# Performance work log

Hardware: AMD Instinct MI355X
Metric: run time of the kernel (lower is better)

Reference implementation:

```python
import jax, jax.numpy as jnp
import numpy as np

B, DIN, E, H, V = 1024, 512, 512, 1024, 4096
MAX_LEN = 32  # max_len=33 with force_eos=True -> 32 decode steps


def setup_inputs() -> dict:
    key = jax.random.key(0)
    ks = jax.random.split(key, 12)
    def u(k, shape, fan_in):
        s = 1.0 / np.sqrt(fan_in)
        return jax.random.uniform(k, shape, jnp.float32, -s, s)
    return {
        "x": jax.random.normal(ks[0], (B, DIN), jnp.float32),
        "W_agent": u(ks[1], (DIN, H), DIN),
        "b_agent": u(ks[2], (H,), DIN),
        "sos_embedding": 0.01 * jax.random.normal(ks[3], (E,), jnp.float32),
        "emb": jax.random.normal(ks[4], (V, E), jnp.float32),
        "W_ih": u(ks[5], (E, H), H),
        "W_hh": u(ks[6], (H, H), H),
        "b_ih": u(ks[7], (H,), H),
        "b_hh": u(ks[8], (H,), H),
        "W_out": u(ks[9], (H, V), H),
        "b_out": u(ks[10], (V,), H),
    }


def reference(x, W_agent, b_agent, sos_embedding, emb, W_ih, W_hh, b_ih, b_hh, W_out, b_out):
    h0 = x @ W_agent + b_agent                      # agent(x): [B, H]
    inp0 = jnp.broadcast_to(sos_embedding, (x.shape[0], E))

    def step(carry, _):
        inp, h = carry
        h = jnp.tanh(inp @ W_ih + h @ W_hh + b_ih + b_hh)   # RNNCell
        logp = jax.nn.log_softmax(h @ W_out + b_out, axis=1)  # [B, V]
        tok = jnp.argmax(logp, axis=1)                      # eval-mode sample
        lp = jnp.take_along_axis(logp, tok[:, None], axis=1)[:, 0]
        ent = -jnp.sum(jnp.exp(logp) * logp, axis=1)
        return (emb[tok], h), (tok, lp, ent)

    (_, _), (seq, lps, ents) = jax.lax.scan(step, (inp0, h0), None, length=MAX_LEN)
    seq = seq.T        # [B, MAX_LEN]
    lps = lps.T
    ents = ents.T
    # force_eos: append zero column
    zf = jnp.zeros((seq.shape[0], 1), jnp.float32)
    sequence = jnp.concatenate([seq, zf.astype(seq.dtype)], axis=1)
    logits = jnp.concatenate([lps, zf], axis=1)
    entropy = jnp.concatenate([ents, zf], axis=1)
    return sequence, logits, entropy
```

## Files before the change

kernel.cpp:

```cpp
#include <hip/hip_runtime.h>
#include <math.h>

#define B_   1024
#define DIN  512
#define EMB  512
#define H_   1024
#define V_   4096
#define TSTEPS 32
#define LEN  33

typedef __attribute__((ext_vector_type(8))) short short8_t;
typedef __attribute__((ext_vector_type(4))) float f32x4;

#define AH_P  131072
#define AI_P  65536
#define B3_P  196608
#define BPO_P 524288

__device__ inline unsigned short bf16_rne(float f) {
  unsigned u = __builtin_bit_cast(unsigned, f);
  u += 0x7FFFu + ((u >> 16) & 1u);
  return (unsigned short)(u >> 16);
}
__device__ inline float bf16_to_f(unsigned short h) {
  unsigned u = ((unsigned)h) << 16;
  return __builtin_bit_cast(float, u);
}
struct S3 { short a, b, c; };
__device__ inline S3 split3(float w) {
  unsigned short h0 = bf16_rne(w);  float r1 = w - bf16_to_f(h0);
  unsigned short h1 = bf16_rne(r1); float r2 = r1 - bf16_to_f(h1);
  S3 r; r.a = (short)h0; r.b = (short)h1; r.c = (short)bf16_rne(r2);
  return r;
}

#define T2MERGE(M1,I1,M2,I2, o1,oi1,o2,oi2)                              \
  if (o1 > M1 || (o1 == M1 && oi1 < I1)) {                               \
    float _n2; int _ni2;                                                 \
    if (M1 > o2 || (M1 == o2 && I1 < oi2)) { _n2 = M1; _ni2 = I1; }      \
    else { _n2 = o2; _ni2 = oi2; }                                       \
    M1 = o1; I1 = oi1; M2 = _n2; I2 = _ni2;                              \
  } else if (o1 > M2 || (o1 == M2 && oi1 < I2)) { M2 = o1; I2 = oi1; }

#define GBT 4
#define GKC 256
__global__ __launch_bounds__(256) void k_gemm(
    float* __restrict__ out,
    const float* __restrict__ A1, int K1, const float* __restrict__ W1,
    const float* __restrict__ A2, int K2, const float* __restrict__ W2,
    const float* __restrict__ b1, const float* __restrict__ b2,
    int do_tanh)
{
  const int N = H_;
  __shared__ float sA[GBT][GKC];
  const int tid = threadIdx.x;
  const int bid = blockIdx.x;
  const int colb = (bid & 7) >> 1;
  const int rowb = ((bid >> 3) << 1) | (bid & 1);
  const int rb  = rowb * GBT;
  const int col = colb * 256 + tid;

  float acc[GBT];
  float bias = b1[col] + (b2 ? b2[col] : 0.0f);
#pragma unroll
  for (int r = 0; r < GBT; ++r) acc[r] = bias;

  const int nch = (K1 + K2) / GKC;
  for (int c = 0; c < nch; ++c) {
    const int kb = c * GKC;
    const float* A; const float* W; int k0, strideA;
    if (kb < K1) { A = A1; W = W1; k0 = kb;      strideA = K1; }
    else         { A = A2; W = W2; k0 = kb - K1; strideA = K2; }
    __syncthreads();
    {
      int r = tid >> 6, kk = (tid & 63) << 2;
      *(float4*)&sA[r][kk] = *(const float4*)(A + (size_t)(rb + r) * strideA + k0 + kk);
    }
    __syncthreads();
    const float* Wp = W + (size_t)k0 * N + col;
#pragma unroll 4
    for (int k = 0; k < GKC; k += 4) {
      float4 a0 = *(const float4*)&sA[0][k];
      float4 a1 = *(const float4*)&sA[1][k];
      float4 a2 = *(const float4*)&sA[2][k];
      float4 a3 = *(const float4*)&sA[3][k];
      float w0 = Wp[(size_t)k * N];
      float w1 = Wp[(size_t)(k + 1) * N];
      float w2 = Wp[(size_t)(k + 2) * N];
      float w3 = Wp[(size_t)(k + 3) * N];
      acc[0] = fmaf(a0.x, w0, acc[0]); acc[1] = fmaf(a1.x, w0, acc[1]);
      acc[2] = fmaf(a2.x, w0, acc[2]); acc[3] = fmaf(a3.x, w0, acc[3]);
      acc[0] = fmaf(a0.y, w1, acc[0]); acc[1] = fmaf(a1.y, w1, acc[1]);
      acc[2] = fmaf(a2.y, w1, acc[2]); acc[3] = fmaf(a3.y, w1, acc[3]);
      acc[0] = fmaf(a0.z, w2, acc[0]); acc[1] = fmaf(a1.z, w2, acc[1]);
      acc[2] = fmaf(a2.z, w2, acc[2]); acc[3] = fmaf(a3.z, w2, acc[3]);
      acc[0] = fmaf(a0.w, w3, acc[0]); acc[1] = fmaf(a1.w, w3, acc[1]);
      acc[2] = fmaf(a2.w, w3, acc[2]); acc[3] = fmaf(a3.w, w3, acc[3]);
    }
  }
#pragma unroll
  for (int r = 0; r < GBT; ++r) {
    float v = acc[r];
    if (do_tanh) v = tanhf(v);
    out[(size_t)(rb + r) * N + col] = v;
  }
}

__global__ __launch_bounds__(256) void k_prepack(
    const float* __restrict__ W, unsigned short* __restrict__ Bp)
{
  int t = blockIdx.x * 256 + threadIdx.x;
  int lane = t & 63;
  int ntg  = (t >> 6) & 255;
  int ks   = t >> 14;
  int col  = ntg * 16 + (lane & 15);
  int krow = ks * 32 + ((lane >> 4) << 3);
  short8_t hv, lv;
#pragma unroll
  for (int j = 0; j < 8; ++j) {
    float w = W[(size_t)(krow + j) * V_ + col];
    unsigned short h = bf16_rne(w);
    hv[j] = (short)h;
    lv[j] = (short)bf16_rne(w - bf16_to_f(h));
  }
  size_t base = ((size_t)ks * 256 + ntg) * 64 + lane;
  short8_t* o = (short8_t*)Bp;
  o[base]         = hv;
  o[base + BPO_P] = lv;
}

__global__ __launch_bounds__(256) void k_packW3(
    const float* __restrict__ Wih, const float* __restrict__ Whh,
    unsigned short* __restrict__ BU)
{
  int t = blockIdx.x * 256 + threadIdx.x;
  int lane = t & 63;
  int ntg  = (t >> 6) & 63;
  int ks   = t >> 12;
  int col  = ntg * 16 + (lane & 15);
  int krow = ks * 32 + ((lane >> 4) << 3);
  short8_t p0, p1, p2;
#pragma unroll
  for (int j = 0; j < 8; ++j) {
    int kr = krow + j;
    float w = (kr < DIN) ? Wih[(size_t)kr * H_ + col]
                         : Whh[(size_t)(kr - DIN) * H_ + col];
    S3 s = split3(w);
    p0[j] = s.a; p1[j] = s.b; p2[j] = s.c;
  }
  short8_t* o = (short8_t*)BU;
  size_t base = ((size_t)ks * 64 + ntg) * 64 + lane;
  o[base] = p0; o[base + B3_P] = p1; o[base + 2 * B3_P] = p2;
}

__global__ __launch_bounds__(256) void k_wtrans(
    const float* __restrict__ W, float* __restrict__ WT)
{
  __shared__ float tile[64][65];
  int kb = (blockIdx.x & 15) * 64;
  int vb = (blockIdx.x >> 4) * 64;
  int t = threadIdx.x;
  {
    int vv = t & 63, k0 = (t >> 6) * 16;
    for (int j = 0; j < 16; ++j)
      tile[k0 + j][vv] = W[(size_t)(kb + k0 + j) * V_ + vb + vv];
  }
  __syncthreads();
  {
    int kk = t & 63, v0 = (t >> 6) * 16;
    for (int j = 0; j < 16; ++j)
      WT[(size_t)(vb + v0 + j) * H_ + kb + kk] = tile[kk][v0 + j];
  }
}

__global__ __launch_bounds__(256) void k_packh(
    const float* __restrict__ h, unsigned short* __restrict__ AU)
{
  int t = blockIdx.x * 256 + threadIdx.x;
  int r = t >> 7, q = t & 127;
  int ks = q >> 2, kg = q & 3;
  int lanep = (r & 15) + (kg << 4);
  int rt = r >> 4;
  const float* src = h + (size_t)r * H_ + q * 8;
  float4 f0 = *(const float4*)src;
  float4 f1 = *(const float4*)(src + 4);
  float f[8] = {f0.x, f0.y, f0.z, f0.w, f1.x, f1.y, f1.z, f1.w};
  short8_t p0, p1, p2;
#pragma unroll
  for (int j = 0; j < 8; ++j) {
    S3 s = split3(f[j]);
    p0[j] = s.a; p1[j] = s.b; p2[j] = s.c;
  }
  short8_t* o = (short8_t*)AU;
  size_t base = (size_t)rt * 2048 + (size_t)ks * 64 + lanep;
  o[base] = p0; o[base + AH_P] = p1; o[base + 2 * AH_P] = p2;
}

__global__ __launch_bounds__(256) void k_sos3(
    const float* __restrict__ sos, unsigned short* __restrict__ AU)
{
  int wid = threadIdx.x >> 6, lane = threadIdx.x & 63;
  int row = blockIdx.x * 4 + wid;
  const float* src = sos + lane * 8;
  float4 f0 = *(const float4*)src;
  float4 f1 = *(const float4*)(src + 4);
  float f[8] = {f0.x, f0.y, f0.z, f0.w, f1.x, f1.y, f1.z, f1.w};
  short8_t p0, p1, p2;
#pragma unroll
  for (int j = 0; j < 8; ++j) {
    S3 s = split3(f[j]);
    p0[j] = s.a; p1[j] = s.b; p2[j] = s.c;
  }
  int ks = lane >> 2, kg = lane & 3;
  int lanep = (row & 15) + (kg << 4);
  int rt = row >> 4;
  short8_t* o = (short8_t*)AU;
  size_t base = (size_t)rt * 1024 + (size_t)ks * 64 + lanep;
  o[base] = p0; o[base + AI_P] = p1; o[base + 2 * AI_P] = p2;
}

__global__ __launch_bounds__(512) void k_rnn(
    const unsigned short* __restrict__ AinpU, const unsigned short* __restrict__ AhU,
    const unsigned short* __restrict__ Bw3U,
    const float* __restrict__ b1, const float* __restrict__ b2,
    float* __restrict__ hout, unsigned short* __restrict__ AhOutU)
{
  __shared__ float sh[64][65];
  const short8_t* Ainp = (const short8_t*)AinpU;
  const short8_t* Ah   = (const short8_t*)AhU;
  const short8_t* Bw3  = (const short8_t*)Bw3U;

  const int bid  = blockIdx.x;
  const int colb = ((bid & 7) << 1) | ((bid >> 3) & 1);
  const int rowb = bid >> 4;
  const int tid  = threadIdx.x, lane = tid & 63, wid = tid >> 6;
  const int wm = (wid >> 1) & 1, wn = wid & 1, kh = wid >> 2;
  const int l15 = lane & 15, lg = lane >> 4;

  f32x4 acc[2][2];
#pragma unroll
  for (int rt = 0; rt < 2; ++rt)
#pragma unroll
    for (int nt = 0; nt < 2; ++nt) {
      int col = colb * 64 + wn * 32 + nt * 16 + l15;
      float b = (kh == 0) ? (b1[col] + b2[col]) : 0.0f;
      acc[rt][nt] = (f32x4){b, b, b, b};
    }

  const int rt0 = rowb * 4 + wm * 2;
  const int ng0 = colb * 4 + wn * 2;
  const int ks0 = kh * 24;

#define RNN_LOAD(A_, B_, KS)                                                   \
  {                                                                            \
    int _ks = (KS);                                                            \
    if (_ks < 16) {                                                            \
      _Pragma("unroll") for (int rt = 0; rt < 2; ++rt)                         \
        _Pragma("unroll") for (int p = 0; p < 3; ++p)                          \
          A_[rt][p] = Ainp[(size_t)p * AI_P + (size_t)(rt0 + rt) * 1024 +      \
                           (size_t)_ks * 64 + lane];                           \
    } else {                                                                   \
      int _h = _ks - 16;                                                       \
      _Pragma("unroll") for (int rt = 0; rt < 2; ++rt)                         \
        _Pragma("unroll") for (int p = 0; p < 3; ++p)                          \
          A_[rt][p] = Ah[(size_t)p * AH_P + (size_t)(rt0 + rt) * 2048 +        \
                         (size_t)_h * 64 + lane];                              \
    }                                                                          \
    _Pragma("unroll") for (int nt = 0; nt < 2; ++nt)                           \
      _Pragma("unroll") for (int p = 0; p < 3; ++p)                            \
        B_[nt][p] = Bw3[(size_t)p * B3_P + (size_t)_ks * 4096 +                \
                        (size_t)(ng0 + nt) * 64 + lane];                       \
  }

  short8_t a[2][3], bb[2][3];
  RNN_LOAD(a, bb, ks0)
#pragma unroll
  for (int i = 0; i < 24; ++i) {
    short8_t an[2][3], bn[2][3];
    if (i < 23) RNN_LOAD(an, bn, ks0 + i + 1)
#pragma unroll
    for (int rt = 0; rt < 2; ++rt)
#pragma unroll
      for (int nt = 0; nt < 2; ++nt) {
        acc[rt][nt] = __builtin_amdgcn_mfma_f32_16x16x32_bf16(a[rt][0], bb[nt][0], acc[rt][nt], 0, 0, 0);
        acc[rt][nt] = __builtin_amdgcn_mfma_f32_16x16x32_bf16(a[rt][0], bb[nt][1], acc[rt][nt], 0, 0, 0);
        acc[rt][nt] = __builtin_amdgcn_mfma_f32_16x16x32_bf16(a[rt][1], bb[nt][0], acc[rt][nt], 0, 0, 0);
        acc[rt][nt] = __builtin_amdgcn_mfma_f32_16x16x32_bf16(a[rt][1], bb[nt][1], acc[rt][nt], 0, 0, 0);
        acc[rt][nt] = __builtin_amdgcn_mfma_f32_16x16x32_bf16(a[rt][0], bb[nt][2], acc[rt][nt], 0, 0, 0);
        acc[rt][nt] = __builtin_amdgcn_mfma_f32_16x16x32_bf16(a[rt][2], bb[nt][0], acc[rt][nt], 0, 0, 0);
      }
    if (i < 23) {
#pragma unroll
      for (int rt = 0; rt < 2; ++rt)
#pragma unroll
        for (int p = 0; p < 3; ++p) { a[rt][p] = an[rt][p]; bb[rt][p] = bn[rt][p]; }
    }
  }
#undef RNN_LOAD

  if (kh == 1) {
#pragma unroll
    for (int rt = 0; rt < 2; ++rt)
#pragma unroll
      for (int nt = 0; nt < 2; ++nt)
#pragma unroll
        for (int r = 0; r < 4; ++r)
          sh[wm * 32 + rt * 16 + lg * 4 + r][wn * 32 + nt * 16 + l15] = acc[rt][nt][r];
  }
  __syncthreads();
  if (kh == 0) {
#pragma unroll
    for (int rt = 0; rt < 2; ++rt)
#pragma unroll
      for (int nt = 0; nt < 2; ++nt)
#pragma unroll
        for (int r = 0; r < 4; ++r) {
          int lr = wm * 32 + rt * 16 + lg * 4 + r;
          int lc = wn * 32 + nt * 16 + l15;
          float v = tanhf(acc[rt][nt][r] + sh[lr][lc]);
          hout[(size_t)(rowb * 64 + lr) * H_ + colb * 64 + lc] = v;
          sh[lr][lc] = v;
        }
  }
  __syncthreads();
  {
    int lr = tid >> 3, q = tid & 7;
    int gk = colb * 64 + q * 8;
    int ks = gk >> 5, kg = (gk >> 3) & 3;
    int gr = rowb * 64 + lr;
    int lanep = (gr & 15) + (kg << 4);
    int rt = gr >> 4;
    short8_t p0, p1, p2;
#pragma unroll
    for (int j = 0; j < 8; ++j) {
      S3 s = split3(sh[lr][q * 8 + j]);
      p0[j] = s.a; p1[j] = s.b; p2[j] = s.c;
    }
    short8_t* o = (short8_t*)AhOutU;
    size_t base = (size_t)rt * 2048 + (size_t)ks * 64 + lanep;
    o[base] = p0; o[base + AH_P] = p1; o[base + 2 * AH_P] = p2;
  }
}

__global__ __launch_bounds__(256) void k_logits3(
    const unsigned short* __restrict__ AhU, const unsigned short* __restrict__ BpU,
    const float* __restrict__ bout, float4* __restrict__ partA,
    float4* __restrict__ partB)
{
  __shared__ float sred[2][2][32][6];
  __shared__ float sbmax[64];
  const short8_t* Ah = (const short8_t*)AhU;
  const short8_t* Bp = (const short8_t*)BpU;

  const int bid  = blockIdx.x;
  const int colb = ((bid & 7) << 2) | ((bid >> 3) & 3);
  const int rowb = bid >> 5;
  const int tid  = threadIdx.x, lane = tid & 63, wid = tid >> 6;
  const int wm = wid >> 1, wn = wid & 1;
  const int l15 = lane & 15, lg = lane >> 4;

  const int colbase = colb * 128 + wn * 64;
  f32x4 acc[2][4];
#pragma unroll
  for (int nt = 0; nt < 4; ++nt) {
    float b = bout[colbase + nt * 16 + l15];
    acc[0][nt] = (f32x4){b, b, b, b};
    acc[1][nt] = acc[0][nt];
  }
  const int rt0 = rowb * 4 + wm * 2;
  const int ng0 = colb * 8 + wn * 4;

#define LG_LOAD(A_, B_, KS)                                                    \
  {                                                                            \
    int _ks = (KS);                                                            \
    _Pragma("unroll") for (int rt = 0; rt < 2; ++rt)                           \
      _Pragma("unroll") for (int p = 0; p < 2; ++p)                            \
        A_[rt][p] = Ah[(size_t)p * AH_P + (size_t)(rt0 + rt) * 2048 +          \
                       (size_t)_ks * 64 + lane];                               \
    _Pragma("unroll") for (int nt = 0; nt < 4; ++nt)                           \
      _Pragma("unroll") for (int p = 0; p < 2; ++p)                            \
        B_[nt][p] = Bp[(size_t)p * BPO_P + ((size_t)_ks * 256 + ng0 + nt) * 64 \
                       + lane];                                                \
  }

  short8_t a[2][2], bb[4][2];
  LG_LOAD(a, bb, 0)
  for (int ks = 0; ks < 32; ++ks) {
    short8_t an[2][2], bn[4][2];
    if (ks < 31) LG_LOAD(an, bn, ks + 1)
#pragma unroll
    for (int rt = 0; rt < 2; ++rt)
#pragma unroll
      for (int nt = 0; nt < 4; ++nt) {
        acc[rt][nt] = __builtin_amdgcn_mfma_f32_16x16x32_bf16(a[rt][0], bb[nt][0], acc[rt][nt], 0, 0, 0);
        acc[rt][nt] = __builtin_amdgcn_mfma_f32_16x16x32_bf16(a[rt][0], bb[nt][1], acc[rt][nt], 0, 0, 0);
        acc[rt][nt] = __builtin_amdgcn_mfma_f32_16x16x32_bf16(a[rt][1], bb[nt][0], acc[rt][nt], 0, 0, 0);
      }
    if (ks < 31) {
#pragma unroll
      for (int rt = 0; rt < 2; ++rt)
#pragma unroll
        for (int p = 0; p < 2; ++p) a[rt][p] = an[rt][p];
#pragma unroll
      for (int nt = 0; nt < 4; ++nt)
#pragma unroll
        for (int p = 0; p < 2; ++p) bb[nt][p] = bn[nt][p];
    }
  }
#undef LG_LOAD

#pragma unroll
  for (int rt = 0; rt < 2; ++rt)
#pragma unroll
    for (int r = 0; r < 4; ++r) {
      float M1 = -1e30f, M2 = -1e30f; int I1 = 0, I2 = 0;
#pragma unroll
      for (int nt = 0; nt < 4; ++nt) {
        float v = acc[rt][nt][r]; int c = colbase + nt * 16 + l15;
        if (v > M1) { M2 = M1; I2 = I1; M1 = v; I1 = c; }
        else if (v > M2) { M2 = v; I2 = c; }
      }
#pragma unroll
      for (int d = 1; d < 16; d <<= 1) {
        float o1 = __shfl_xor(M1, d); int oi1 = __shfl_xor(I1, d);
        float o2 = __shfl_xor(M2, d); int oi2 = __shfl_xor(I2, d);
        T2MERGE(M1, I1, M2, I2, o1, oi1, o2, oi2)
      }
      if (l15 == 0) {
        int rl = rt * 16 + lg * 4 + r;
        sred[wm][wn][rl][0] = M1; sred[wm][wn][rl][1] = (float)I1;
        sred[wm][wn][rl][2] = M2; sred[wm][wn][rl][3] = (float)I2;
      }
    }
  __syncthreads();
  if (tid < 64) {
    int wmm = tid >> 5, rl = tid & 31;
    float M1 = sred[wmm][0][rl][0]; int I1 = (int)sred[wmm][0][rl][1];
    float M2 = sred[wmm][0][rl][2]; int I2 = (int)sred[wmm][0][rl][3];
    float o1 = sred[wmm][1][rl][0]; int oi1 = (int)sred[wmm][1][rl][1];
    float o2 = sred[wmm][1][rl][2]; int oi2 = (int)sred[wmm][1][rl][3];
    T2MERGE(M1, I1, M2, I2, o1, oi1, o2, oi2)
    int row = rowb * 64 + wmm * 32 + rl;
    partA[(size_t)row * 32 + colb] = make_float4(M1, (float)I1, M2, (float)I2);
    sbmax[wmm * 32 + rl] = M1;
  }
  __syncthreads();
#pragma unroll
  for (int rt = 0; rt < 2; ++rt)
#pragma unroll
    for (int r = 0; r < 4; ++r) {
      float m = sbmax[wm * 32 + rt * 16 + lg * 4 + r];
      float s = 0.f, tsum = 0.f;
#pragma unroll
      for (int nt = 0; nt < 4; ++nt) {
        float d = acc[rt][nt][r] - m;
        float e = expf(d);
        s += e; tsum += d * e;
      }
#pragma unroll
      for (int d = 1; d < 16; d <<= 1) { s += __shfl_xor(s, d); tsum += __shfl_xor(tsum, d); }
      if (l15 == 0) {
        int rl = rt * 16 + lg * 4 + r;
        sred[wm][wn][rl][4] = s; sred[wm][wn][rl][5] = tsum;
      }
    }
  __syncthreads();
  if (tid < 64) {
    int wmm = tid >> 5, rl = tid & 31;
    float s = sred[wmm][0][rl][4] + sred[wmm][1][rl][4];
    float tsum = sred[wmm][0][rl][5] + sred[wmm][1][rl][5];
    int row = rowb * 64 + wmm * 32 + rl;
    partB[(size_t)row * 32 + colb] = make_float4(s, tsum, 0.f, 0.f);
  }
}

__global__ __launch_bounds__(256) void k_finalize3(
    const float4* __restrict__ partA, const float4* __restrict__ partB,
    const float* __restrict__ h, const float* __restrict__ Wout,
    const float* __restrict__ WoutT, const float* __restrict__ bout,
    const float* __restrict__ emb, float* __restrict__ out,
    unsigned short* __restrict__ AinpU, int tstep)
{
  const int lane = threadIdx.x & 63;
  const int wid  = threadIdx.x >> 6;
  const int row  = blockIdx.x * 4 + wid;

  float M1 = -1e30f, M2 = -1e30f; int I1 = 0, I2 = 0;
  float bm = -1e30f, s_l = 0.f, t_l = 0.f;
  if (lane < 32) {
    float4 pa = partA[(size_t)row * 32 + lane];
    float4 pb = partB[(size_t)row * 32 + lane];
    M1 = pa.x; I1 = (int)pa.y; M2 = pa.z; I2 = (int)pa.w;
    bm = pa.x; s_l = pb.x; t_l = pb.y;
  }
  for (int d = 1; d < 32; d <<= 1) {
    float o1 = __shfl_xor(M1, d); int oi1 = __shfl_xor(I1, d);
    float o2 = __shfl_xor(M2, d); int oi2 = __shfl_xor(I2, d);
    T2MERGE(M1, I1, M2, I2, o1, oi1, o2, oi2)
  }
  M1 = __shfl(M1, 0); I1 = __shfl(I1, 0);
  M2 = __shfl(M2, 0); I2 = __shfl(I2, 0);

  float e = (lane < 32) ? expf(bm - M1) : 0.f;
  float s = e * s_l;
  float tsum = e * (t_l + (bm - M1) * s_l);
  for (int d = 1; d < 64; d <<= 1) { s += __shfl_xor(s, d); tsum += __shfl_xor(tsum, d); }

  const float* hrow = h + (size_t)row * H_;
  float d1 = 0.f, d2 = 0.f;
  if (WoutT) {
    const float* w1 = WoutT + (size_t)I1 * H_;
    const float* w2 = WoutT + (size_t)I2 * H_;
#pragma unroll 4
    for (int k = lane; k < H_; k += 64) {
      float hv = hrow[k];
      d1 = fmaf(hv, w1[k], d1);
      d2 = fmaf(hv, w2[k], d2);
    }
  } else {
    for (int k = lane; k < H_; k += 64) {
      float hv = hrow[k];
      d1 = fmaf(hv, Wout[(size_t)k * V_ + I1], d1);
      d2 = fmaf(hv, Wout[(size_t)k * V_ + I2], d2);
    }
  }
  for (int d = 1; d < 64; d <<= 1) { d1 += __shfl_xor(d1, d); d2 += __shfl_xor(d2, d); }
  d1 += bout[I1]; d2 += bout[I2];

  int tok; float ltok;
  if (d2 > d1 || (d2 == d1 && I2 < I1)) { tok = I2; ltok = d2; }
  else                                  { tok = I1; ltok = d1; }
  float lg_s = logf(s);
  if (lane == 0) {
    out[(size_t)row * LEN + tstep]                  = (float)tok;
    out[(size_t)(B_ * LEN) + row * LEN + tstep]     = ltok - M1 - lg_s;
    out[(size_t)(2 * B_ * LEN) + row * LEN + tstep] = lg_s - tsum / s;
  }
  const float* er = emb + (size_t)tok * EMB + lane * 8;
  float4 f0 = *(const float4*)er;
  float4 f1 = *(const float4*)(er + 4);
  float f[8] = {f0.x, f0.y, f0.z, f0.w, f1.x, f1.y, f1.z, f1.w};
  short8_t p0, p1, p2;
#pragma unroll
  for (int j = 0; j < 8; ++j) {
    S3 s3v = split3(f[j]);
    p0[j] = s3v.a; p1[j] = s3v.b; p2[j] = s3v.c;
  }
  int ks = lane >> 2, kg = lane & 3;
  int lanep = (row & 15) + (kg << 4);
  int rt = row >> 4;
  short8_t* o = (short8_t*)AinpU;
  size_t base = (size_t)rt * 1024 + (size_t)ks * 64 + lanep;
  o[base] = p0; o[base + AI_P] = p1; o[base + 2 * AI_P] = p2;
}

#define BT 16
#define KC 128
__global__ __launch_bounds__(256) void k_logits_f32(
    const float* __restrict__ h, const float* __restrict__ Wout,
    const float* __restrict__ bout, float4* __restrict__ part)
{
  __shared__ float sA[BT][KC];
  __shared__ float redf[4][BT];
  __shared__ float redf2[4][BT];
  __shared__ int   redi[4][BT];
  __shared__ float bm[BT];

  const int tid = threadIdx.x;
  const int rb  = blockIdx.x * BT;
  const int c0  = blockIdx.y * 512 + tid * 2;

  float acc[BT][2];
  float2 bj = *(const float2*)(bout + c0);
#pragma unroll
  for (int r = 0; r < BT; ++r) { acc[r][0] = bj.x; acc[r][1] = bj.y; }

  for (int kb = 0; kb < H_; kb += KC) {
    __syncthreads();
    {
      float4* s4 = (float4*)sA;
#pragma unroll
      for (int i = 0; i < 2; ++i) {
        int idx = tid + i * 256;
        int r = idx >> 5, kk = (idx & 31) << 2;
        s4[idx] = *(const float4*)(h + (size_t)(rb + r) * H_ + kb + kk);
      }
    }
    __syncthreads();
    const float* Wp = Wout + (size_t)kb * V_ + c0;
#pragma unroll 2
    for (int k = 0; k < KC; k += 4) {
      float4 a[BT];
#pragma unroll
      for (int r = 0; r < BT; ++r) a[r] = *((const float4*)sA[r] + (k >> 2));
      float2 w[4];
#pragma unroll
      for (int u = 0; u < 4; ++u) w[u] = *(const float2*)(Wp + (size_t)(k + u) * V_);
#pragma unroll
      for (int u = 0; u < 4; ++u)
#pragma unroll
        for (int r = 0; r < BT; ++r) {
          float av = ((const float*)&a[r])[u];
          acc[r][0] = fmaf(av, w[u].x, acc[r][0]);
          acc[r][1] = fmaf(av, w[u].y, acc[r][1]);
        }
    }
  }

  const int wid = tid >> 6, lane = tid & 63;
  float mx[BT]; int ix[BT];
#pragma unroll
  for (int r = 0; r < BT; ++r) {
    float m = acc[r][0]; int ii = c0;
    if (acc[r][1] > m) { m = acc[r][1]; ii = c0 + 1; }
    mx[r] = m; ix[r] = ii;
  }
#pragma unroll
  for (int r = 0; r < BT; ++r) {
    for (int d = 32; d; d >>= 1) {
      float ov = __shfl_xor(mx[r], d);
      int   oi = __shfl_xor(ix[r], d);
      if (ov > mx[r] || (ov == mx[r] && oi < ix[r])) { mx[r] = ov; ix[r] = oi; }
    }
  }
  if (lane == 0) {
#pragma unroll
    for (int r = 0; r < BT; ++r) { redf[wid][r] = mx[r]; redi[wid][r] = ix[r]; }
  }
  __syncthreads();
  if (tid < BT) {
    float m = redf[0][tid]; int ii = redi[0][tid];
    for (int w = 1; w < 4; ++w) {
      float ov = redf[w][tid]; int oi = redi[w][tid];
      if (ov > m || (ov == m && oi < ii)) { m = ov; ii = oi; }
    }
    bm[tid] = m; redi[0][tid] = ii;
  }
  __syncthreads();
  float ss[BT], tt[BT];
#pragma unroll
  for (int r = 0; r < BT; ++r) {
    float m = bm[r];
    float s = 0.f, t = 0.f;
#pragma unroll
    for (int j = 0; j < 2; ++j) {
      float d = acc[r][j] - m;
      float e2 = expf(d);
      s += e2; t += d * e2;
    }
    ss[r] = s; tt[r] = t;
  }
#pragma unroll
  for (int r = 0; r < BT; ++r) {
    for (int d = 32; d; d >>= 1) {
      ss[r] += __shfl_xor(ss[r], d);
      tt[r] += __shfl_xor(tt[r], d);
    }
  }
  if (lane == 0) {
#pragma unroll
    for (int r = 0; r < BT; ++r) { redf[wid][r] = ss[r]; redf2[wid][r] = tt[r]; }
  }
  __syncthreads();
  if (tid < BT) {
    float s = 0.f, t = 0.f;
    for (int w = 0; w < 4; ++w) { s += redf[w][tid]; t += redf2[w][tid]; }
    part[(size_t)(rb + tid) * 8 + blockIdx.y] =
        make_float4(bm[tid], s, t, (float)redi[0][tid]);
  }
}

__global__ __launch_bounds__(128) void k_finalize_f32(
    const float4* __restrict__ part, const float* __restrict__ emb,
    float* __restrict__ out, float* __restrict__ inp, int t)
{
  const int row = blockIdx.x;
  __shared__ int s_tok;
  if (threadIdx.x == 0) {
    float4 p[8];
#pragma unroll
    for (int i = 0; i < 8; ++i) p[i] = part[(size_t)row * 8 + i];
    float m = p[0].x; int tok = (int)p[0].w;
#pragma unroll
    for (int i = 1; i < 8; ++i)
      if (p[i].x > m) { m = p[i].x; tok = (int)p[i].w; }
    float S = 0.f, T = 0.f;
#pragma unroll
    for (int i = 0; i < 8; ++i) {
      float w = expf(p[i].x - m);
      S += w * p[i].y;
      T += w * (p[i].z + (p[i].x - m) * p[i].y);
    }
    float lp  = -logf(S);
    float ent = logf(S) - T / S;
    out[(size_t)row * LEN + t]                  = (float)tok;
    out[(size_t)(B_ * LEN) + row * LEN + t]     = lp;
    out[(size_t)(2 * B_ * LEN) + row * LEN + t] = ent;
    s_tok = tok;
  }
  __syncthreads();
  const float4* src = (const float4*)(emb + (size_t)s_tok * EMB);
  float4* dst = (float4*)(inp + (size_t)row * EMB);
  for (int i = threadIdx.x; i < EMB / 4; i += blockDim.x) dst[i] = src[i];
}

__global__ void k_sos(const float* __restrict__ sos, float* __restrict__ inp) {
  int i = blockIdx.x * blockDim.x + threadIdx.x;
  ((float4*)inp)[i] = ((const float4*)sos)[i & (EMB / 4 - 1)];
}
__global__ void k_zero(float* __restrict__ out) {
  int i = blockIdx.x * blockDim.x + threadIdx.x;
  if (i < 3 * B_) {
    int sec = i >> 10, row = i & (B_ - 1);
    out[(size_t)sec * (B_ * LEN) + (size_t)row * LEN + (LEN - 1)] = 0.f;
  }
}

extern "C" void kernel_launch(void* const* d_in, const int* in_sizes, int n_in,
                              void* d_out, int out_size, void* d_ws, size_t ws_size,
                              hipStream_t stream) {
  const float* x       = (const float*)d_in[0];
  const float* W_agent = (const float*)d_in[1];
  const float* b_agent = (const float*)d_in[2];
  const float* sos     = (const float*)d_in[3];
  const float* emb     = (const float*)d_in[4];
  const float* W_ih    = (const float*)d_in[5];
  const float* W_hh    = (const float*)d_in[6];
  const float* b_ih    = (const float*)d_in[7];
  const float* b_hh    = (const float*)d_in[8];
  const float* W_out   = (const float*)d_in[9];
  const float* b_out   = (const float*)d_in[10];
  float* out = (float*)d_out;

  const size_t SZ_BPOUT = 16777216;
  const size_t SZ_BW3   = 9437184;
  const size_t SZ_WT    = 16777216;
  const size_t SZ_AH    = 6291456;
  const size_t SZ_AINP  = 3145728;
  const size_t SZ_H     = 4194304;
  const size_t SZ_PART  = 524288;
  const size_t NEED_A = SZ_BPOUT + SZ_BW3 + SZ_WT + 2 * SZ_AH + SZ_AINP + SZ_H + 2 * SZ_PART;
  const size_t NEED_B = NEED_A - SZ_WT;

  if (ws_size >= NEED_B) {
    const bool useT = ws_size >= NEED_A;
    char* p = (char*)d_ws;
    unsigned short* BpOut = (unsigned short*)p; p += SZ_BPOUT;
    unsigned short* Bw3   = (unsigned short*)p; p += SZ_BW3;
    float* WoutT = nullptr;
    if (useT) { WoutT = (float*)p; p += SZ_WT; }
    unsigned short* Ah0  = (unsigned short*)p; p += SZ_AH;
    unsigned short* Ah1  = (unsigned short*)p; p += SZ_AH;
    unsigned short* Ainp = (unsigned short*)p; p += SZ_AINP;
    float*  hbuf  = (float*)p; p += SZ_H;
    float4* partA = (float4*)p; p += SZ_PART;
    float4* partB = (float4*)p;

    k_sos3<<<dim3(256), dim3(256), 0, stream>>>(sos, Ainp);
    k_prepack<<<dim3(2048), dim3(256), 0, stream>>>(W_out, BpOut);
    k_packW3<<<dim3(768), dim3(256), 0, stream>>>(W_ih, W_hh, Bw3);
    if (useT) k_wtrans<<<dim3(1024), dim3(256), 0, stream>>>(W_out, WoutT);
    k_gemm<<<dim3(1024), dim3(256), 0, stream>>>(
        hbuf, x, DIN, W_agent, nullptr, 0, nullptr, b_agent, nullptr, 0);
    k_packh<<<dim3(512), dim3(256), 0, stream>>>(hbuf, Ah0);

    for (int t = 0; t < TSTEPS; ++t) {
      unsigned short* AhIn  = (t & 1) ? Ah1 : Ah0;
      unsigned short* AhOut = (t & 1) ? Ah0 : Ah1;
      k_rnn<<<dim3(256), dim3(512), 0, stream>>>(
          Ainp, AhIn, Bw3, b_ih, b_hh, hbuf, AhOut);
      k_logits3<<<dim3(512), dim3(256), 0, stream>>>(
          AhOut, BpOut, b_out, partA, partB);
      k_finalize3<<<dim3(256), dim3(256), 0, stream>>>(
          partA, partB, hbuf, W_out, WoutT, b_out, emb, out, Ainp, t);
    }
  } else {
    float*  h0buf = (float*)d_ws;
    float*  h1buf = h0buf + (size_t)B_ * H_;
    float*  inp   = h1buf + (size_t)B_ * H_;
    float4* part  = (float4*)(inp + (size_t)B_ * EMB);

    k_sos<<<dim3(B_ * EMB / 4 / 256), dim3(256), 0, stream>>>(sos, inp);
    k_gemm<<<dim3(1024), dim3(256), 0, stream>>>(
        h0buf, x, DIN, W_agent, nullptr, 0, nullptr, b_agent, nullptr, 0);
    for (int t = 0; t < TSTEPS; ++t) {
      float* hr = (t & 1) ? h1buf : h0buf;
      float* hw = (t & 1) ? h0buf : h1buf;
      k_gemm<<<dim3(1024), dim3(256), 0, stream>>>(
          hw, inp, EMB, W_ih, hr, H_, W_hh, b_ih, b_hh, 1);
      k_logits_f32<<<dim3(B_ / BT, V_ / 512), dim3(256), 0, stream>>>(
          hw, W_out, b_out, part);
      k_finalize_f32<<<dim3(B_), dim3(128), 0, stream>>>(part, emb, out, inp, t);
    }
  }
  k_zero<<<dim3(12), dim3(256), 0, stream>>>(out);
}
```

Baseline: 2.334 ms.

## Use single bf16 pass for output projection and triple-buffer operand loads

The output logits GEMM no longer uses the split-bf16 (hi/lo) scheme with three MFMAs per tile. It packs W_out and reads the hidden-state activations as a single bf16 pass. This cuts MFMA work and operand traffic to a third or less, and halves the packed W_out buffer. The load pipeline also moves from double to triple buffering with a fully unrolled k-loop. The risk is lower logit precision, which can change argmax token choices and the log-prob and entropy values compared with the fp32 reference.

```diff
diff --git a/kernel.cpp b/kernel.cpp
--- a/kernel.cpp
+++ b/kernel.cpp
@@ -15,7 +15,6 @@
 #define AH_P  131072
 #define AI_P  65536
 #define B3_P  196608
-#define BPO_P 524288
 
 __device__ inline unsigned short bf16_rne(float f) {
   unsigned u = __builtin_bit_cast(unsigned, f);
@@ -115,18 +114,14 @@
   int ks   = t >> 14;
   int col  = ntg * 16 + (lane & 15);
   int krow = ks * 32 + ((lane >> 4) << 3);
-  short8_t hv, lv;
+  short8_t hv;
 #pragma unroll
   for (int j = 0; j < 8; ++j) {
     float w = W[(size_t)(krow + j) * V_ + col];
-    unsigned short h = bf16_rne(w);
-    hv[j] = (short)h;
-    lv[j] = (short)bf16_rne(w - bf16_to_f(h));
+    hv[j] = (short)bf16_rne(w);
   }
   size_t base = ((size_t)ks * 256 + ntg) * 64 + lane;
-  short8_t* o = (short8_t*)Bp;
-  o[base]         = hv;
-  o[base + BPO_P] = lv;
+  ((short8_t*)Bp)[base] = hv;
 }
 
 __global__ __launch_bounds__(256) void k_packW3(
@@ -374,38 +369,24 @@
   {                                                                            \
     int _ks = (KS);                                                            \
     _Pragma("unroll") for (int rt = 0; rt < 2; ++rt)                           \
-      _Pragma("unroll") for (int p = 0; p < 2; ++p)                            \
-        A_[rt][p] = Ah[(size_t)p * AH_P + (size_t)(rt0 + rt) * 2048 +          \
-                       (size_t)_ks * 64 + lane];                               \
+      A_[rt] = Ah[(size_t)(rt0 + rt) * 2048 + (size_t)_ks * 64 + lane];        \
     _Pragma("unroll") for (int nt = 0; nt < 4; ++nt)                           \
-      _Pragma("unroll") for (int p = 0; p < 2; ++p)                            \
-        B_[nt][p] = Bp[(size_t)p * BPO_P + ((size_t)_ks * 256 + ng0 + nt) * 64 \
-                       + lane];                                                \
-  }
-
-  short8_t a[2][2], bb[4][2];
-  LG_LOAD(a, bb, 0)
+      B_[nt] = Bp[((size_t)_ks * 256 + ng0 + nt) * 64 + lane];                 \
+  }
+
+  short8_t abuf[3][2], bbuf[3][4];
+  LG_LOAD(abuf[0], bbuf[0], 0)
+  LG_LOAD(abuf[1], bbuf[1], 1)
+#pragma unroll
   for (int ks = 0; ks < 32; ++ks) {
-    short8_t an[2][2], bn[4][2];
-    if (ks < 31) LG_LOAD(an, bn, ks + 1)
+    const int cur = ks % 3, nxt = (ks + 2) % 3;
+    if (ks + 2 < 32) LG_LOAD(abuf[nxt], bbuf[nxt], ks + 2)
 #pragma unroll
     for (int rt = 0; rt < 2; ++rt)
 #pragma unroll
-      for (int nt = 0; nt < 4; ++nt) {
-        acc[rt][nt] = __builtin_amdgcn_mfma_f32_16x16x32_bf16(a[rt][0], bb[nt][0], acc[rt][nt], 0, 0, 0);
-        acc[rt][nt] = __builtin_amdgcn_mfma_f32_16x16x32_bf16(a[rt][0], bb[nt][1], acc[rt][nt], 0, 0, 0);
-        acc[rt][nt] = __builtin_amdgcn_mfma_f32_16x16x32_bf16(a[rt][1], bb[nt][0], acc[rt][nt], 0, 0, 0);
-      }
-    if (ks < 31) {
-#pragma unroll
-      for (int rt = 0; rt < 2; ++rt)
-#pragma unroll
-        for (int p = 0; p < 2; ++p) a[rt][p] = an[rt][p];
-#pragma unroll
       for (int nt = 0; nt < 4; ++nt)
-#pragma unroll
-        for (int p = 0; p < 2; ++p) bb[nt][p] = bn[nt][p];
-    }
+        acc[rt][nt] = __builtin_amdgcn_mfma_f32_16x16x32_bf16(
+            abuf[cur][rt], bbuf[cur][nt], acc[rt][nt], 0, 0, 0);
   }
 #undef LG_LOAD
 
@@ -732,7 +713,7 @@
   const float* b_out   = (const float*)d_in[10];
   float* out = (float*)d_out;
 
-  const size_t SZ_BPOUT = 16777216;
+  const size_t SZ_BPOUT = 8388608;
   const size_t SZ_BW3   = 9437184;
   const size_t SZ_WT    = 16777216;
   const size_t SZ_AH    = 6291456;
```

Result: faster. 1.943 ms (-16.7%).
